# Kernel tuning notes

Measured on AMD Instinct MI355X. Metric: run time of the kernel, lower is better.

Reference implementation:

```python
import jax, jax.numpy as jnp
import numpy as np

HIDDEN = 1280
NUM_HEADS = 16
HEAD_DIM = HIDDEN // NUM_HEADS  # 80
ROPE_DIM = HEAD_DIM // 2        # 40
THETA = 10000.0
SEQ = 3072


def setup_inputs() -> dict:
    key = jax.random.key(0)
    ks = jax.random.split(key, 6)
    hidden_states = jax.random.normal(ks[0], (SEQ, HIDDEN), dtype=jnp.float32)
    position_ids = jax.random.randint(ks[1], (SEQ, 2), 0, 64, dtype=jnp.int32)
    qkv_w = jax.random.normal(ks[2], (HIDDEN, 3 * HIDDEN), dtype=jnp.float32) * (HIDDEN ** -0.5)
    qkv_b = jax.random.normal(ks[3], (3 * HIDDEN,), dtype=jnp.float32) * 0.02
    o_w = jax.random.normal(ks[4], (HIDDEN, HIDDEN), dtype=jnp.float32) * (HIDDEN ** -0.5)
    o_b = jax.random.normal(ks[5], (HIDDEN,), dtype=jnp.float32) * 0.02
    return {"hidden_states": hidden_states, "position_ids": position_ids,
            "qkv_w": qkv_w, "qkv_b": qkv_b, "o_w": o_w, "o_b": o_b}


def _rotate_half(x):
    x1, x2 = jnp.split(x, 2, axis=-1)
    return jnp.concatenate([-x2, x1], axis=-1)


def reference(hidden_states, position_ids, qkv_w, qkv_b, o_w, o_b):
    seq_len = hidden_states.shape[0]
    # fused QKV projection
    qkv = hidden_states @ qkv_w + qkv_b                     # (S, 3*H*D)
    qkv = qkv.reshape(seq_len, 3, NUM_HEADS, HEAD_DIM)
    q, k, v = qkv[:, 0], qkv[:, 1], qkv[:, 2]               # each (S, h, d)
    # 2D RoPE: inv_freq over rope dim = head_dim // 2
    inv_freq = 1.0 / (THETA ** (jnp.arange(0, ROPE_DIM, 2, dtype=jnp.float32) / ROPE_DIM))
    pos = position_ids.astype(jnp.float32)
    h_freqs = jnp.outer(pos[:, 0], inv_freq)                # (S, rope/2)
    w_freqs = jnp.outer(pos[:, 1], inv_freq)                # (S, rope/2)
    freqs = jnp.concatenate([h_freqs, w_freqs], axis=-1)    # (S, rope)
    emb = jnp.concatenate([freqs, freqs], axis=-1)          # (S, head_dim)
    cos = jnp.cos(emb)[:, None, :]                          # (S, 1, d)
    sin = jnp.sin(emb)[:, None, :]
    q = q * cos + _rotate_half(q) * sin
    k = k * cos + _rotate_half(k) * sin
    # manual attention
    scaling = HEAD_DIM ** -0.5
    attn = jnp.einsum('qhd,khd->hqk', q * scaling, k)       # (h, S, S)
    attn = jax.nn.softmax(attn, axis=-1)
    out = jnp.einsum('hqk,khd->qhd', attn, v)               # (S, h, d)
    out = out.reshape(seq_len, HIDDEN)
    return out @ o_w + o_b
```

## Files before the change

### kernel.cpp

```cpp
#include <hip/hip_runtime.h>

#define SEQ  3072
#define HID  1280
#define NH   16
#define HD   80
#define NQKV 3840
#define KSP  2

typedef unsigned short u16;
typedef unsigned int u32;
typedef __attribute__((ext_vector_type(8))) short short8;
typedef __attribute__((ext_vector_type(4))) short short4v;
typedef __attribute__((ext_vector_type(4))) float floatx4;
typedef __attribute__((ext_vector_type(4))) unsigned int uint4v;

__device__ __forceinline__ u16 f2bf(float x) {
    u32 u = __float_as_uint(x);
    u += 0x7fffu + ((u >> 16) & 1u);
    return (u16)(u >> 16);
}
__device__ __forceinline__ u32 packrne(float a, float b) {
    return (u32)f2bf(a) | ((u32)f2bf(b) << 16);
}

typedef const __attribute__((address_space(1))) unsigned int* gp1_t;
typedef __attribute__((address_space(3))) unsigned int* lp3_t;
__device__ __forceinline__ void gld16(const void* g, void* l) {
    __builtin_amdgcn_global_load_lds((gp1_t)g, (lp3_t)l, 16, 0, 0);
}

__device__ __forceinline__ int swz80(int c, int r) {
    return (c < 8) ? (c ^ (r & 7)) : (8 + ((c - 8) ^ ((r >> 2) & 1)));
}

__global__ void prep_k(const int* __restrict__ pos, float* __restrict__ cosb,
                       float* __restrict__ sinb, const float* __restrict__ hs,
                       u16* __restrict__ hH, const float* __restrict__ qkvw,
                       u16* __restrict__ wT, const float* __restrict__ ow,
                       u16* __restrict__ owT) {
    __shared__ float tile[32][33];
    const int b = blockIdx.x, t = threadIdx.x;
    if (b < 480) {
        int i = b * 256 + t;
        int s = i / 40, j = i % 40;
        float p = (float)((j < 20) ? pos[s * 2] : pos[s * 2 + 1]);
        int k = (j < 20) ? j : j - 20;
        float inv = powf(10000.0f, -(float)k / 20.0f);
        float a = p * inv;
        cosb[s * 40 + j] = cosf(a);
        sinb[s * 40 + j] = sinf(a);
    } else if (b < 4320) {
        int i = (b - 480) * 256 + t;
        const float4 x = ((const float4*)hs)[i];
        uint2 o;
        o.x = packrne(x.x, x.y);
        o.y = packrne(x.z, x.w);
        ((uint2*)hH)[i] = o;
    } else {
        const float* w;
        u16* dst;
        int K, N, nx, ky;
        if (b < 9120) {
            int i = b - 4320;
            nx = i % 120; ky = i / 120; w = qkvw; dst = wT; K = HID; N = NQKV;
        } else {
            int i = b - 9120;
            nx = i % 40; ky = i / 40; w = ow; dst = owT; K = HID; N = HID;
        }
        int n0 = nx * 32, k0 = ky * 32;
        int c = t & 31, r8 = t >> 5;
        for (int rr = r8; rr < 32; rr += 8)
            tile[rr][c] = w[(size_t)(k0 + rr) * N + n0 + c];
        __syncthreads();
        for (int rr = r8; rr < 32; rr += 8)
            dst[(size_t)(n0 + rr) * K + k0 + c] = f2bf(tile[c][rr]);
    }
}

__global__ __launch_bounds__(256, 3) void gemm_bf16_k(
    const u16* __restrict__ A, const u16* __restrict__ B,
    const float* __restrict__ bias, float* __restrict__ C,
    int M, int N, int K, int mode) {
    __shared__ u16 lA[128 * 64], lB[128 * 64];
    const int t = threadIdx.x, lane = t & 63, w = t >> 6;
    const int qi = lane & 15, quad = lane >> 4;
    int id = blockIdx.x;
    int xcd = id & 7, sN = id >> 3;
    int m_idx, n_idx;
    if (mode == 0) {
        n_idx = (xcd & 1) * 15 + sN % 15;
        m_idx = (xcd >> 1) * 6 + sN / 15;
    } else {
        m_idx = xcd * 3 + sN / 10;
        n_idx = sN % 10;
    }
    const int m0 = m_idx * 128, n0 = n_idx * 128;
    const int wm = (w >> 1) * 64, wn = (w & 1) * 64;

    floatx4 acc[4][4];
    for (int mi = 0; mi < 4; mi++)
        for (int ni = 0; ni < 4; ni++) acc[mi][ni] = (floatx4){0.f, 0.f, 0.f, 0.f};

    const int rg = lane >> 3;
    const int ce = ((lane & 7) ^ rg) * 8;
    size_t gA[4], gB[4];
    for (int g = 0; g < 4; g++) {
        int row = w * 32 + g * 8 + rg;
        gA[g] = (size_t)(m0 + row) * K + ce;
        gB[g] = (size_t)(n0 + row) * K + ce;
    }

    for (int k0 = 0; k0 < K; k0 += 64) {
        for (int g = 0; g < 4; g++) {
            gld16(A + gA[g] + k0, &lA[(w * 32 + g * 8) * 64]);
            gld16(B + gB[g] + k0, &lB[(w * 32 + g * 8) * 64]);
        }
        __syncthreads();
        short8 af[4][2], bf[4][2];
        for (int mi = 0; mi < 4; mi++) {
            int row = wm + mi * 16 + qi;
            for (int kh = 0; kh < 2; kh++)
                af[mi][kh] = *(const short8*)&lA[row * 64 + (((kh * 4 + quad) ^ (row & 7)) << 3)];
        }
        for (int ni = 0; ni < 4; ni++) {
            int row = wn + ni * 16 + qi;
            for (int kh = 0; kh < 2; kh++)
                bf[ni][kh] = *(const short8*)&lB[row * 64 + (((kh * 4 + quad) ^ (row & 7)) << 3)];
        }
        for (int mi = 0; mi < 4; mi++)
            for (int ni = 0; ni < 4; ni++) {
                acc[mi][ni] = __builtin_amdgcn_mfma_f32_16x16x32_bf16(af[mi][0], bf[ni][0], acc[mi][ni], 0, 0, 0);
                acc[mi][ni] = __builtin_amdgcn_mfma_f32_16x16x32_bf16(af[mi][1], bf[ni][1], acc[mi][ni], 0, 0, 0);
            }
        __syncthreads();
    }
    for (int mi = 0; mi < 4; mi++)
        for (int ni = 0; ni < 4; ni++) {
            int col = n0 + wn + ni * 16 + qi;
            int rowb = m0 + wm + mi * 16 + quad * 4;
            float b = bias[col];
            for (int r = 0; r < 4; r++)
                C[(size_t)(rowb + r) * N + col] = acc[mi][ni][r] + b;
        }
}

__global__ void pack_qkv_k(const float* __restrict__ qkv, const float* __restrict__ cosb,
                           const float* __restrict__ sinb,
                           u16* __restrict__ Qs, u16* __restrict__ Ks, u16* __restrict__ Vs) {
    __shared__ float lv[80 * 65];
    const int t = threadIdx.x;
    const int h = blockIdx.y, s0 = blockIdx.x * 64;
    const float qsc = 0.11180339887498949f * 1.4426950408889634f;

    for (int i = t; i < 64 * 10; i += 256) {
        int rl = i / 10, jg = i % 10;
        int s = s0 + rl, j = jg * 4;
        const float4 cc = *(const float4*)&cosb[s * 40 + j];
        const float4 ss = *(const float4*)&sinb[s * 40 + j];
        const float* qb = qkv + (size_t)s * NQKV + h * HD;
        const float4 q1 = *(const float4*)&qb[j];
        const float4 q2 = *(const float4*)&qb[j + 40];
        const float* kb = qb + HID;
        const float4 k1 = *(const float4*)&kb[j];
        const float4 k2 = *(const float4*)&kb[j + 40];
        uint2 qo1, qo2, ko1, ko2;
        qo1.x = packrne((q1.x * cc.x - q2.x * ss.x) * qsc, (q1.y * cc.y - q2.y * ss.y) * qsc);
        qo1.y = packrne((q1.z * cc.z - q2.z * ss.z) * qsc, (q1.w * cc.w - q2.w * ss.w) * qsc);
        qo2.x = packrne((q2.x * cc.x + q1.x * ss.x) * qsc, (q2.y * cc.y + q1.y * ss.y) * qsc);
        qo2.y = packrne((q2.z * cc.z + q1.z * ss.z) * qsc, (q2.w * cc.w + q1.w * ss.w) * qsc);
        ko1.x = packrne(k1.x * cc.x - k2.x * ss.x, k1.y * cc.y - k2.y * ss.y);
        ko1.y = packrne(k1.z * cc.z - k2.z * ss.z, k1.w * cc.w - k2.w * ss.w);
        ko2.x = packrne(k2.x * cc.x + k1.x * ss.x, k2.y * cc.y + k1.y * ss.y);
        ko2.y = packrne(k2.z * cc.z + k1.z * ss.z, k2.w * cc.w + k1.w * ss.w);
        size_t base = (size_t)(h * SEQ + s) * 80;
        int sub0 = j & 7, sub1 = (j + 40) & 7;
        int p0 = swz80(j >> 3, s);
        int p1 = swz80((j + 40) >> 3, s);
        *(uint2*)&Qs[base + p0 * 8 + sub0] = qo1;
        *(uint2*)&Qs[base + p1 * 8 + sub1] = qo2;
        *(uint2*)&Ks[base + p0 * 8 + sub0] = ko1;
        *(uint2*)&Ks[base + p1 * 8 + sub1] = ko2;
    }
    for (int i = t; i < 64 * 80; i += 256) {
        int rl = i / 80, d = i % 80;
        lv[d * 65 + rl] = qkv[(size_t)(s0 + rl) * NQKV + 2 * HID + h * HD + d];
    }
    __syncthreads();
    for (int i = t; i < 80 * 16; i += 256) {
        int d = i / 16, g = i % 16;
        int c2l = g * 4;
        float v0 = lv[d * 65 + c2l], v1 = lv[d * 65 + c2l + 1];
        float v2 = lv[d * 65 + c2l + 2], v3 = lv[d * 65 + c2l + 3];
        int pc = (g >> 1) ^ (d & 7);
        uint2 o;
        o.x = packrne(v0, v1);
        o.y = packrne(v2, v3);
        *(uint2*)&Vs[((size_t)h * HD + d) * SEQ + s0 + pc * 8 + (g & 1) * 4] = o;
    }
}

__global__ __launch_bounds__(256, 3) void attn_k(
    const u16* __restrict__ Qs, const u16* __restrict__ Ks, const u16* __restrict__ Vs,
    float* __restrict__ Op, float* __restrict__ lp) {
    __shared__ u16 kbuf[2][5120];
    __shared__ u16 vbuf[2][5120];

    const int t = threadIdx.x, lane = t & 63, w = t >> 6;
    const int qi = lane & 15, quad = lane >> 4;
    const int h = blockIdx.y, q0 = blockIdx.x * 128, ksp = blockIdx.z;
    const int kc0 = ksp * (SEQ / 2);
    u16* const kflat = &kbuf[0][0];

    {
        const u16* Qt = Qs + (size_t)(h * SEQ + q0) * 80;
        for (int j = 0; j < 5; j++) {
            int o = (w * 5 + j) * 512;
            gld16(Qt + o + lane * 8, kflat + o);
        }
    }
    __syncthreads();
    short8 bq[2][3];
    for (int qg = 0; qg < 2; qg++) {
        const u16* rb = &kflat[(w * 32 + qg * 16 + qi) * 80];
        bq[qg][0] = *(const short8*)&rb[(quad ^ (qi & 7)) << 3];
        bq[qg][1] = *(const short8*)&rb[((4 + quad) ^ (qi & 7)) << 3];
        short4v t2 = *(const short4v*)&rb[((8 + ((quad >> 1) ^ ((qi >> 2) & 1))) << 3) + ((quad & 1) << 2)];
        bq[qg][2] = (short8){t2.x, t2.y, t2.z, t2.w, 0, 0, 0, 0};
    }
    __syncthreads();

    float l_lane[2] = {0.f, 0.f};
    floatx4 acco[2][5];
    for (int qg = 0; qg < 2; qg++)
        for (int dt = 0; dt < 5; dt++) acco[qg][dt] = (floatx4){0.f, 0.f, 0.f, 0.f};

    auto stage = [&](int it, int buf) {
        int kc = kc0 + it * 64;
        const u16* Kt = Ks + (size_t)(h * SEQ + kc) * 80;
        for (int i = w; i < 10; i += 4)
            gld16(Kt + i * 512 + lane * 8, &kbuf[buf][i * 512]);
        const u16* Vt = Vs + (size_t)h * HD * SEQ + kc;
        for (int i = w; i < 10; i += 4) {
            int p16 = i * 64 + lane;
            int d = p16 >> 3, pc = p16 & 7;
            gld16(Vt + (size_t)d * SEQ + pc * 8, &vbuf[buf][i * 512]);
        }
    };
    stage(0, 0);
    __syncthreads();

    const int NT = (SEQ / 2) / 64;
    for (int it = 0; it < NT; it++) {
        int cur = it & 1;
        if (it + 1 < NT) stage(it + 1, cur ^ 1);
        const u16* kb = &kbuf[cur][0];
        const u16* vb = &vbuf[cur][0];
#pragma unroll
        for (int c2 = 0; c2 < 2; c2++) {
            u32 pkx[2][2], pky[2][2];
#pragma unroll
            for (int ktl = 0; ktl < 2; ktl++) {
                int arow = (c2 * 2 + ktl) * 16 + qi;
                const u16* rb = &kb[arow * 80];
                short8 a0 = *(const short8*)&rb[(quad ^ (qi & 7)) << 3];
                short8 a1 = *(const short8*)&rb[((4 + quad) ^ (qi & 7)) << 3];
                short4v a2v = *(const short4v*)&rb[((8 + ((quad >> 1) ^ ((qi >> 2) & 1))) << 3) + ((quad & 1) << 2)];
                short8 a2 = (short8){a2v.x, a2v.y, a2v.z, a2v.w, 0, 0, 0, 0};
#pragma unroll
                for (int qg = 0; qg < 2; qg++) {
                    floatx4 s = (floatx4){0.f, 0.f, 0.f, 0.f};
                    __builtin_amdgcn_s_setprio(1);
                    s = __builtin_amdgcn_mfma_f32_16x16x32_bf16(a0, bq[qg][0], s, 0, 0, 0);
                    s = __builtin_amdgcn_mfma_f32_16x16x32_bf16(a1, bq[qg][1], s, 0, 0, 0);
                    s = __builtin_amdgcn_mfma_f32_16x16x32_bf16(a2, bq[qg][2], s, 0, 0, 0);
                    __builtin_amdgcn_s_setprio(0);
                    float e0 = __builtin_amdgcn_exp2f(s[0]);
                    float e1 = __builtin_amdgcn_exp2f(s[1]);
                    float e2 = __builtin_amdgcn_exp2f(s[2]);
                    float e3 = __builtin_amdgcn_exp2f(s[3]);
                    l_lane[qg] += (e0 + e1) + (e2 + e3);
                    pkx[qg][ktl] = __builtin_amdgcn_perm(__float_as_uint(e1), __float_as_uint(e0), 0x07060302u);
                    pky[qg][ktl] = __builtin_amdgcn_perm(__float_as_uint(e3), __float_as_uint(e2), 0x07060302u);
                }
            }
            short8 bp[2];
#pragma unroll
            for (int qg = 0; qg < 2; qg++) {
                auto s0 = __builtin_amdgcn_permlane32_swap(pkx[qg][0], pkx[qg][1], false, false);
                auto s1 = __builtin_amdgcn_permlane32_swap(pky[qg][0], pky[qg][1], false, false);
                auto t0 = __builtin_amdgcn_permlane16_swap(s0[0], s0[1], false, false);
                auto t1 = __builtin_amdgcn_permlane16_swap(s1[0], s1[1], false, false);
                uint4v bb = (uint4v){t0[0], t1[0], t0[1], t1[1]};
                bp[qg] = __builtin_bit_cast(short8, bb);
            }
            int pv = (4 * c2 + quad) ^ (qi & 7);
            __builtin_amdgcn_s_setprio(1);
#pragma unroll
            for (int dt = 0; dt < 5; dt++) {
                short8 av = *(const short8*)&vb[((dt * 16 + qi) * 8 + pv) * 8];
                acco[0][dt] = __builtin_amdgcn_mfma_f32_16x16x32_bf16(av, bp[0], acco[0][dt], 0, 0, 0);
                acco[1][dt] = __builtin_amdgcn_mfma_f32_16x16x32_bf16(av, bp[1], acco[1][dt], 0, 0, 0);
            }
            __builtin_amdgcn_s_setprio(0);
        }
        __syncthreads();
    }

    for (int qg = 0; qg < 2; qg++) {
        float lq = l_lane[qg];
        lq += __shfl_xor(lq, 16);
        lq += __shfl_xor(lq, 32);
        int q = q0 + w * 32 + qg * 16 + qi;
        if (quad == 0) lp[(size_t)(ksp * NH + h) * SEQ + q] = lq;
        for (int dt = 0; dt < 5; dt++)
            for (int r = 0; r < 4; r++) {
                int d = dt * 16 + quad * 4 + r;
                Op[((size_t)(ksp * NH + h) * HD + d) * SEQ + q] = acco[qg][dt][r];
            }
    }
}

__global__ void merge_k(const float* __restrict__ Op, const float* __restrict__ lp,
                        u16* __restrict__ att) {
    __shared__ float ls[HD * 65];
    __shared__ float li[64];
    const int t = threadIdx.x;
    const int h = blockIdx.y, q0 = blockIdx.x * 64;
    for (int i = t; i < HD * 16; i += 256) {
        int d = i / 16, g = i % 16;
        size_t a0 = ((size_t)h * HD + d) * SEQ + q0 + g * 4;
        size_t a1 = ((size_t)(NH + h) * HD + d) * SEQ + q0 + g * 4;
        const float4 v0 = *(const float4*)&Op[a0];
        const float4 v1 = *(const float4*)&Op[a1];
        ls[d * 65 + g * 4 + 0] = v0.x + v1.x;
        ls[d * 65 + g * 4 + 1] = v0.y + v1.y;
        ls[d * 65 + g * 4 + 2] = v0.z + v1.z;
        ls[d * 65 + g * 4 + 3] = v0.w + v1.w;
    }
    if (t < 64)
        li[t] = 1.0f / (lp[(size_t)h * SEQ + q0 + t] + lp[(size_t)(NH + h) * SEQ + q0 + t]);
    __syncthreads();
    for (int i = t; i < 64 * 40; i += 256) {
        int ql = i / 40, dg = i % 40;
        int d0 = dg * 2;
        float s = li[ql];
        u32 o = packrne(ls[d0 * 65 + ql] * s, ls[(d0 + 1) * 65 + ql] * s);
        *(u32*)&att[(size_t)(q0 + ql) * HID + h * HD + d0] = o;
    }
}

extern "C" void kernel_launch(void* const* d_in, const int* in_sizes, int n_in,
                              void* d_out, int out_size, void* d_ws, size_t ws_size,
                              hipStream_t stream) {
    const float* hs   = (const float*)d_in[0];
    const int*   pos  = (const int*)d_in[1];
    const float* qkvw = (const float*)d_in[2];
    const float* qkvb = (const float*)d_in[3];
    const float* ow   = (const float*)d_in[4];
    const float* ob   = (const float*)d_in[5];
    float* out = (float*)d_out;

    char* p = (char*)d_ws;
    auto alloc = [&](size_t bytes) {
        char* r = p;
        p += (bytes + 255) & ~(size_t)255;
        return r;
    };
    float* cosb = (float*)alloc((size_t)SEQ * 40 * 4);
    float* sinb = (float*)alloc((size_t)SEQ * 40 * 4);
    u16* owT = (u16*)alloc((size_t)HID * HID * 2);
    char* pool1 = alloc(7864320 + 9830400);
    u16* hH = (u16*)pool1;
    u16* wT = (u16*)(pool1 + 7864320);
    u16* Qs = (u16*)pool1;
    u16* Ks = (u16*)(pool1 + 7864320);
    char* pool2 = alloc((size_t)SEQ * NQKV * 4);
    float* qkv_s = (float*)pool2;
    u16* att  = (u16*)pool2;
    float* Op = (float*)(pool2 + 7864320);
    float* lp = (float*)(pool2 + 39321600);
    u16* Vs = (u16*)alloc((size_t)NH * HD * SEQ * 2);

    hipLaunchKernelGGL(prep_k, dim3(10720), dim3(256), 0, stream,
                       pos, cosb, sinb, hs, hH, qkvw, wT, ow, owT);
    hipLaunchKernelGGL(gemm_bf16_k, dim3(720), dim3(256), 0, stream,
                       hH, wT, qkvb, qkv_s, SEQ, NQKV, HID, 0);
    hipLaunchKernelGGL(pack_qkv_k, dim3(SEQ / 64, NH), dim3(256), 0, stream,
                       qkv_s, cosb, sinb, Qs, Ks, Vs);
    hipLaunchKernelGGL(attn_k, dim3(SEQ / 128, NH, 2), dim3(256), 0, stream,
                       Qs, Ks, Vs, Op, lp);
    hipLaunchKernelGGL(merge_k, dim3(SEQ / 64, NH), dim3(256), 0, stream, Op, lp, att);
    hipLaunchKernelGGL(gemm_bf16_k, dim3(240), dim3(256), 0, stream,
                       att, owT, ob, out, SEQ, HID, HID, 1);
}
```

Before: 234.8 us.

## Split attention block into eight waves each owning sixteen query rows

The attention kernel moves from 4 waves handling 32 query rows each to 8 waves handling 16 rows each, with 512 threads per block and a new launch bound. Per-wave accumulator and Q-fragment registers are halved, and K/V staging is spread across 8 waves. The goal is higher occupancy and better latency hiding. The cost is that each K/V tile loaded from LDS now feeds half as many MFMAs per wave, so LDS read traffic per unit of compute doubles.

Result: no change. 234.0 us (-0.3%).

```diff
diff --git a/kernel.cpp b/kernel.cpp
--- a/kernel.cpp
+++ b/kernel.cpp
@@ -199,7 +199,7 @@
     }
 }
 
-__global__ __launch_bounds__(256, 3) void attn_k(
+__global__ __launch_bounds__(512, 6) void attn_k(
     const u16* __restrict__ Qs, const u16* __restrict__ Ks, const u16* __restrict__ Vs,
     float* __restrict__ Op, float* __restrict__ lp) {
     __shared__ u16 kbuf[2][5120];
@@ -213,34 +213,31 @@
 
     {
         const u16* Qt = Qs + (size_t)(h * SEQ + q0) * 80;
-        for (int j = 0; j < 5; j++) {
-            int o = (w * 5 + j) * 512;
-            gld16(Qt + o + lane * 8, kflat + o);
-        }
-    }
-    __syncthreads();
-    short8 bq[2][3];
-    for (int qg = 0; qg < 2; qg++) {
-        const u16* rb = &kflat[(w * 32 + qg * 16 + qi) * 80];
-        bq[qg][0] = *(const short8*)&rb[(quad ^ (qi & 7)) << 3];
-        bq[qg][1] = *(const short8*)&rb[((4 + quad) ^ (qi & 7)) << 3];
+        for (int i = w; i < 20; i += 8)
+            gld16(Qt + i * 512 + lane * 8, kflat + i * 512);
+    }
+    __syncthreads();
+    short8 bq[3];
+    {
+        const u16* rb = &kflat[(w * 16 + qi) * 80];
+        bq[0] = *(const short8*)&rb[(quad ^ (qi & 7)) << 3];
+        bq[1] = *(const short8*)&rb[((4 + quad) ^ (qi & 7)) << 3];
         short4v t2 = *(const short4v*)&rb[((8 + ((quad >> 1) ^ ((qi >> 2) & 1))) << 3) + ((quad & 1) << 2)];
-        bq[qg][2] = (short8){t2.x, t2.y, t2.z, t2.w, 0, 0, 0, 0};
-    }
-    __syncthreads();
-
-    float l_lane[2] = {0.f, 0.f};
-    floatx4 acco[2][5];
-    for (int qg = 0; qg < 2; qg++)
-        for (int dt = 0; dt < 5; dt++) acco[qg][dt] = (floatx4){0.f, 0.f, 0.f, 0.f};
+        bq[2] = (short8){t2.x, t2.y, t2.z, t2.w, 0, 0, 0, 0};
+    }
+    __syncthreads();
+
+    float l_lane = 0.f;
+    floatx4 acco[5];
+    for (int dt = 0; dt < 5; dt++) acco[dt] = (floatx4){0.f, 0.f, 0.f, 0.f};
 
     auto stage = [&](int it, int buf) {
         int kc = kc0 + it * 64;
         const u16* Kt = Ks + (size_t)(h * SEQ + kc) * 80;
-        for (int i = w; i < 10; i += 4)
+        for (int i = w; i < 10; i += 8)
             gld16(Kt + i * 512 + lane * 8, &kbuf[buf][i * 512]);
         const u16* Vt = Vs + (size_t)h * HD * SEQ + kc;
-        for (int i = w; i < 10; i += 4) {
+        for (int i = w; i < 10; i += 8) {
             int p16 = i * 64 + lane;
             int d = p16 >> 3, pc = p16 & 7;
             gld16(Vt + (size_t)d * SEQ + pc * 8, &vbuf[buf][i * 512]);
@@ -257,7 +254,7 @@
         const u16* vb = &vbuf[cur][0];
 #pragma unroll
         for (int c2 = 0; c2 < 2; c2++) {
-            u32 pkx[2][2], pky[2][2];
+            u32 pkx[2], pky[2];
 #pragma unroll
             for (int ktl = 0; ktl < 2; ktl++) {
                 int arow = (c2 * 2 + ktl) * 16 + qi;
@@ -266,56 +263,48 @@
                 short8 a1 = *(const short8*)&rb[((4 + quad) ^ (qi & 7)) << 3];
                 short4v a2v = *(const short4v*)&rb[((8 + ((quad >> 1) ^ ((qi >> 2) & 1))) << 3) + ((quad & 1) << 2)];
                 short8 a2 = (short8){a2v.x, a2v.y, a2v.z, a2v.w, 0, 0, 0, 0};
-#pragma unroll
-                for (int qg = 0; qg < 2; qg++) {
-                    floatx4 s = (floatx4){0.f, 0.f, 0.f, 0.f};
-                    __builtin_amdgcn_s_setprio(1);
-                    s = __builtin_amdgcn_mfma_f32_16x16x32_bf16(a0, bq[qg][0], s, 0, 0, 0);
-                    s = __builtin_amdgcn_mfma_f32_16x16x32_bf16(a1, bq[qg][1], s, 0, 0, 0);
-                    s = __builtin_amdgcn_mfma_f32_16x16x32_bf16(a2, bq[qg][2], s, 0, 0, 0);
-                    __builtin_amdgcn_s_setprio(0);
-                    float e0 = __builtin_amdgcn_exp2f(s[0]);
-                    float e1 = __builtin_amdgcn_exp2f(s[1]);
-                    float e2 = __builtin_amdgcn_exp2f(s[2]);
-                    float e3 = __builtin_amdgcn_exp2f(s[3]);
-                    l_lane[qg] += (e0 + e1) + (e2 + e3);
-                    pkx[qg][ktl] = __builtin_amdgcn_perm(__float_as_uint(e1), __float_as_uint(e0), 0x07060302u);
-                    pky[qg][ktl] = __builtin_amdgcn_perm(__float_as_uint(e3), __float_as_uint(e2), 0x07060302u);
-                }
+                floatx4 s = (floatx4){0.f, 0.f, 0.f, 0.f};
+                __builtin_amdgcn_s_setprio(1);
+                s = __builtin_amdgcn_mfma_f32_16x16x32_bf16(a0, bq[0], s, 0, 0, 0);
+                s = __builtin_amdgcn_mfma_f32_16x16x32_bf16(a1, bq[1], s, 0, 0, 0);
+                s = __builtin_amdgcn_mfma_f32_16x16x32_bf16(a2, bq[2], s, 0, 0, 0);
+                __builtin_amdgcn_s_setprio(0);
+                float e0 = __builtin_amdgcn_exp2f(s[0]);
+                float e1 = __builtin_amdgcn_exp2f(s[1]);
+                float e2 = __builtin_amdgcn_exp2f(s[2]);
+                float e3 = __builtin_amdgcn_exp2f(s[3]);
+                l_lane += (e0 + e1) + (e2 + e3);
+                pkx[ktl] = __builtin_amdgcn_perm(__float_as_uint(e1), __float_as_uint(e0), 0x07060302u);
+                pky[ktl] = __builtin_amdgcn_perm(__float_as_uint(e3), __float_as_uint(e2), 0x07060302u);
             }
-            short8 bp[2];
-#pragma unroll
-            for (int qg = 0; qg < 2; qg++) {
-                auto s0 = __builtin_amdgcn_permlane32_swap(pkx[qg][0], pkx[qg][1], false, false);
-                auto s1 = __builtin_amdgcn_permlane32_swap(pky[qg][0], pky[qg][1], false, false);
-                auto t0 = __builtin_amdgcn_permlane16_swap(s0[0], s0[1], false, false);
-                auto t1 = __builtin_amdgcn_permlane16_swap(s1[0], s1[1], false, false);
-                uint4v bb = (uint4v){t0[0], t1[0], t0[1], t1[1]};
-                bp[qg] = __builtin_bit_cast(short8, bb);
-            }
+            auto s0 = __builtin_amdgcn_permlane32_swap(pkx[0], pkx[1], false, false);
+            auto s1 = __builtin_amdgcn_permlane32_swap(pky[0], pky[1], false, false);
+            auto t0 = __builtin_amdgcn_permlane16_swap(s0[0], s0[1], false, false);
+            auto t1 = __builtin_amdgcn_permlane16_swap(s1[0], s1[1], false, false);
+            uint4v bb = (uint4v){t0[0], t1[0], t0[1], t1[1]};
+            short8 bp = __builtin_bit_cast(short8, bb);
             int pv = (4 * c2 + quad) ^ (qi & 7);
             __builtin_amdgcn_s_setprio(1);
 #pragma unroll
             for (int dt = 0; dt < 5; dt++) {
                 short8 av = *(const short8*)&vb[((dt * 16 + qi) * 8 + pv) * 8];
-                acco[0][dt] = __builtin_amdgcn_mfma_f32_16x16x32_bf16(av, bp[0], acco[0][dt], 0, 0, 0);
-                acco[1][dt] = __builtin_amdgcn_mfma_f32_16x16x32_bf16(av, bp[1], acco[1][dt], 0, 0, 0);
+                acco[dt] = __builtin_amdgcn_mfma_f32_16x16x32_bf16(av, bp, acco[dt], 0, 0, 0);
             }
             __builtin_amdgcn_s_setprio(0);
         }
         __syncthreads();
     }
 
-    for (int qg = 0; qg < 2; qg++) {
-        float lq = l_lane[qg];
+    {
+        float lq = l_lane;
         lq += __shfl_xor(lq, 16);
         lq += __shfl_xor(lq, 32);
-        int q = q0 + w * 32 + qg * 16 + qi;
+        int q = q0 + w * 16 + qi;
         if (quad == 0) lp[(size_t)(ksp * NH + h) * SEQ + q] = lq;
         for (int dt = 0; dt < 5; dt++)
             for (int r = 0; r < 4; r++) {
                 int d = dt * 16 + quad * 4 + r;
-                Op[((size_t)(ksp * NH + h) * HD + d) * SEQ + q] = acco[qg][dt][r];
+                Op[((size_t)(ksp * NH + h) * HD + d) * SEQ + q] = acco[dt][r];
             }
     }
 }
@@ -387,7 +376,7 @@
                        hH, wT, qkvb, qkv_s, SEQ, NQKV, HID, 0);
     hipLaunchKernelGGL(pack_qkv_k, dim3(SEQ / 64, NH), dim3(256), 0, stream,
                        qkv_s, cosb, sinb, Qs, Ks, Vs);
-    hipLaunchKernelGGL(attn_k, dim3(SEQ / 128, NH, 2), dim3(256), 0, stream,
+    hipLaunchKernelGGL(attn_k, dim3(SEQ / 128, NH, 2), dim3(512), 0, stream,
                        Qs, Ks, Vs, Op, lp);
     hipLaunchKernelGGL(merge_k, dim3(SEQ / 64, NH), dim3(256), 0, stream, Op, lp, att);
     hipLaunchKernelGGL(gemm_bf16_k, dim3(240), dim3(256), 0, stream,
```
